# Kernel optimization log

Hardware: AMD Instinct MI355X
Metric: run time of the kernel (lower is better)

## Reference

```python
import jax, jax.numpy as jnp
import numpy as np

B, N, F = 8, 1024, 512
H, D = 4, 128  # num_heads, output_dim
LEAKY_ALPHA = 0.2
MASK_VAL = -1e10


def setup_inputs() -> dict:
    key = jax.random.key(0)
    ks = jax.random.split(key, 6)
    X = jax.random.normal(ks[0], (B, N, F), dtype=jnp.float32)
    A = (jax.random.uniform(ks[1], (B, N, N)) < 0.05).astype(jnp.float32)
    A = jnp.maximum(A, jnp.eye(N, dtype=jnp.float32)[None])
    W_att = jax.random.normal(ks[2], (H, F, D), dtype=jnp.float32) * (1.0 / np.sqrt(F))
    a_att = jax.random.normal(ks[3], (H, 2, D), dtype=jnp.float32) * (1.0 / np.sqrt(D))
    kernel = jax.random.normal(ks[4], (H, F, D), dtype=jnp.float32) * (1.0 / np.sqrt(F))
    bias = jax.random.normal(ks[5], (H * D,), dtype=jnp.float32) * 0.02
    return {"X": X, "A": A, "W_att": W_att, "a_att": a_att, "kernel": kernel, "bias": bias}


def reference(X, A, W_att, a_att, kernel, bias):
    # Per-head feature projection used only for attention scores: [H,B,N,D]
    xf = jnp.einsum('bnf,hfd->hbnd', X, W_att)
    att_self = jnp.einsum('hbnd,hd->hbn', xf, a_att[:, 0])       # [H,B,N]
    att_neigh = jnp.einsum('hbnd,hd->hbn', xf, a_att[:, 1])      # [H,B,N]
    # additive scores: scores[h,b,i,j] = self[i] + neigh[j]
    scores = att_self[..., :, None] + att_neigh[..., None, :]    # [H,B,N,N]
    scores = jnp.where(scores >= 0, scores, LEAKY_ALPHA * scores)
    scores = scores + MASK_VAL * (1.0 - A)[None]                 # adjacency mask
    attn = jax.nn.softmax(scores, axis=-1)                       # [H,B,N,N]
    # aggregate raw features X, then per-head kernel projection
    agg = jnp.einsum('hbij,bjf->hbif', attn, X)                  # [H,B,N,F]
    out = jnp.einsum('hbnf,hfd->bnhd', agg, kernel)              # [B,N,H,D]
    out = out.reshape(out.shape[0], out.shape[1], -1)            # concat heads -> [B,N,H*D]
    out = out + bias
    return jax.nn.elu(out)
```

## Files before the change

kernel.cpp:

```cpp
#include <hip/hip_runtime.h>
#include <hip/hip_bf16.h>
#include <math.h>

namespace {
constexpr int B = 8, N = 1024, F = 512, H = 4, D = 128, HD = H * D;
constexpr int ROWS = B * N;
constexpr float LEAKY = 0.2f;

constexpr size_t UV_OFF  = 0;
constexpr size_t ATT_OFF = 4096;
constexpr size_t Y_OFF   = 69632;
constexpr size_t XB_OFF  = 2166784;
constexpr size_t WKB_OFF = 4263936;
}

typedef __attribute__((ext_vector_type(8))) short short8;
typedef __attribute__((ext_vector_type(4))) float f32x4;
typedef __attribute__((ext_vector_type(2))) float f32x2;

__device__ __forceinline__ ushort bf16bits(float x) {
    __hip_bfloat16 h = __float2bfloat16(x);
    return *reinterpret_cast<ushort*>(&h);
}
__device__ __forceinline__ float blo(uint u) {
    return __uint_as_float(u << 16);
}
__device__ __forceinline__ float bhi(uint u) {
    return __uint_as_float(u & 0xffff0000u);
}

extern "C" __global__ __launch_bounds__(256) void k_pre(
    const float* __restrict__ Watt, const float* __restrict__ aatt,
    const float* __restrict__ Wk, float* __restrict__ uv,
    __hip_bfloat16* __restrict__ Wkb) {
    __shared__ ushort T[128][136];
    if (blockIdx.x < 16) {
        int h = blockIdx.x >> 2, f0 = (blockIdx.x & 3) * 128;
#pragma unroll
        for (int p = 0; p < 16; ++p) {
            int fi = p * 8 + (threadIdx.x >> 5);
            int d4 = (threadIdx.x & 31) * 4;
            float4 v = *reinterpret_cast<const float4*>(
                Wk + ((size_t)h * F + f0 + fi) * D + d4);
            T[d4 + 0][fi] = bf16bits(v.x);
            T[d4 + 1][fi] = bf16bits(v.y);
            T[d4 + 2][fi] = bf16bits(v.z);
            T[d4 + 3][fi] = bf16bits(v.w);
        }
        __syncthreads();
        int d = threadIdx.x >> 1, hf = threadIdx.x & 1;
        ushort* dst =
            (ushort*)Wkb + (size_t)(h * 128 + d) * F + f0 + hf * 64;
        const ushort* src = &T[d][hf * 64];
#pragma unroll
        for (int q = 0; q < 8; ++q)
            *reinterpret_cast<uint4*>(dst + q * 8) =
                *reinterpret_cast<const uint4*>(src + q * 8);
    } else {
        int t = (blockIdx.x - 16) * 256 + threadIdx.x;
        int f = t % F;
        int h = (t / F) % H;
        int w = t / (F * H);
        const float* Wrow = Watt + (size_t)(h * F + f) * D;
        const float* arow = aatt + (size_t)(h * 2 + w) * D;
        float s = 0.f;
#pragma unroll 4
        for (int d = 0; d < D; ++d) s = fmaf(Wrow[d], arow[d], s);
        uv[(size_t)w * (H * F) + h * F + f] = s;
    }
}

extern "C" __global__ __launch_bounds__(256) void k_att(
    const float* __restrict__ X, const float* __restrict__ uv,
    float* __restrict__ att, __hip_bfloat16* __restrict__ Xb) {
    int wave = threadIdx.x >> 6, lane = threadIdx.x & 63;
    int row = blockIdx.x * 4 + wave;
    const float4* xr = reinterpret_cast<const float4*>(X + (size_t)row * F);
    float4 v0 = xr[lane * 2], v1 = xr[lane * 2 + 1];

    union { short8 s; ushort u[8]; } pk;
    pk.u[0] = bf16bits(v0.x); pk.u[1] = bf16bits(v0.y);
    pk.u[2] = bf16bits(v0.z); pk.u[3] = bf16bits(v0.w);
    pk.u[4] = bf16bits(v1.x); pk.u[5] = bf16bits(v1.y);
    pk.u[6] = bf16bits(v1.z); pk.u[7] = bf16bits(v1.w);
    *reinterpret_cast<short8*>(Xb + (size_t)row * F + lane * 8) = pk.s;

    float acc[2][H];
#pragma unroll
    for (int w = 0; w < 2; ++w)
#pragma unroll
        for (int h = 0; h < H; ++h) {
            const float4* up = reinterpret_cast<const float4*>(
                uv + (size_t)w * (H * F) + h * F + lane * 8);
            float4 u0 = up[0], u1 = up[1];
            float a = 0.f;
            a = fmaf(v0.x, u0.x, a); a = fmaf(v0.y, u0.y, a);
            a = fmaf(v0.z, u0.z, a); a = fmaf(v0.w, u0.w, a);
            a = fmaf(v1.x, u1.x, a); a = fmaf(v1.y, u1.y, a);
            a = fmaf(v1.z, u1.z, a); a = fmaf(v1.w, u1.w, a);
            acc[w][h] = a;
        }
#pragma unroll
    for (int w = 0; w < 2; ++w)
#pragma unroll
        for (int h = 0; h < H; ++h) {
            float v = acc[w][h];
#pragma unroll
            for (int off = 32; off > 0; off >>= 1) v += __shfl_xor(v, off);
            if (lane == 0) att[(size_t)w * (H * ROWS) + h * ROWS + row] = v;
        }
}

extern "C" __global__ __launch_bounds__(256) void k_gemm(
    const __hip_bfloat16* __restrict__ Xb,
    const __hip_bfloat16* __restrict__ Wkb,
    __hip_bfloat16* __restrict__ Y) {
    __shared__ __align__(16) char smem[24576];
    int tid = threadIdx.x;
    int lane = tid & 63, wv = tid >> 6;
    int wr = wv >> 1, wc = wv & 1;
    int lt = (blockIdx.x & 7) * 64 + (blockIdx.x >> 3);
    int bm = lt >> 3, bn = lt & 7;
    int row0 = bm * 128, col0 = bn * 64;

    const ushort* Ag = (const ushort*)Xb;
    const ushort* Bg = (const ushort*)Wkb;

    int aoff[4][2], boff[2][2];
#pragma unroll
    for (int ks = 0; ks < 2; ++ks) {
        int cb = ks * 4 + (lane >> 4);
#pragma unroll
        for (int mi = 0; mi < 4; ++mi) {
            int ra = wr * 64 + mi * 16 + (lane & 15);
            aoff[mi][ks] = ra * 128 + (cb ^ (ra & 7)) * 16;
        }
#pragma unroll
        for (int ni = 0; ni < 2; ++ni) {
            int rb = wc * 32 + ni * 16 + (lane & 15);
            boff[ni][ks] = 16384 + rb * 128 + (cb ^ (rb & 7)) * 16;
        }
    }
    int srowA[4], sgbA[4], srowB[2], sgbB[2];
#pragma unroll
    for (int i = 0; i < 4; ++i) {
        srowA[i] = i * 32 + wv * 8 + (lane >> 3);
        sgbA[i] = (lane & 7) ^ (srowA[i] & 7);
    }
#pragma unroll
    for (int i = 0; i < 2; ++i) {
        srowB[i] = i * 32 + wv * 8 + (lane >> 3);
        sgbB[i] = (lane & 7) ^ (srowB[i] & 7);
    }

    f32x4 acc[4][2] = {};
    for (int k0 = 0; k0 < F; k0 += 64) {
        __syncthreads();
#pragma unroll
        for (int i = 0; i < 4; ++i) {
            const ushort* ga = Ag + (size_t)(row0 + srowA[i]) * F + k0 + sgbA[i] * 8;
            __builtin_amdgcn_global_load_lds(
                (const __attribute__((address_space(1))) uint32_t*)ga,
                (__attribute__((address_space(3))) uint32_t*)(smem + i * 4096 + wv * 1024),
                16, 0, 0);
        }
#pragma unroll
        for (int i = 0; i < 2; ++i) {
            const ushort* gb = Bg + (size_t)(col0 + srowB[i]) * F + k0 + sgbB[i] * 8;
            __builtin_amdgcn_global_load_lds(
                (const __attribute__((address_space(1))) uint32_t*)gb,
                (__attribute__((address_space(3))) uint32_t*)(smem + 16384 + i * 4096 + wv * 1024),
                16, 0, 0);
        }
        __syncthreads();
#pragma unroll
        for (int ks = 0; ks < 2; ++ks) {
            short8 af[4], bf[2];
#pragma unroll
            for (int mi = 0; mi < 4; ++mi)
                af[mi] = *reinterpret_cast<short8*>(smem + aoff[mi][ks]);
#pragma unroll
            for (int ni = 0; ni < 2; ++ni)
                bf[ni] = *reinterpret_cast<short8*>(smem + boff[ni][ks]);
#pragma unroll
            for (int mi = 0; mi < 4; ++mi)
#pragma unroll
                for (int ni = 0; ni < 2; ++ni)
                    acc[mi][ni] = __builtin_amdgcn_mfma_f32_16x16x32_bf16(
                        af[mi], bf[ni], acc[mi][ni], 0, 0, 0);
        }
    }
    int cr = (lane >> 4) * 4, cc = lane & 15;
#pragma unroll
    for (int mi = 0; mi < 4; ++mi)
#pragma unroll
        for (int ni = 0; ni < 2; ++ni) {
            int gr = row0 + wr * 64 + mi * 16 + cr;
            int gc = col0 + wc * 32 + ni * 16 + cc;
#pragma unroll
            for (int r = 0; r < 4; ++r)
                Y[(size_t)(gr + r) * HD + gc] =
                    __float2bfloat16(acc[mi][ni][r]);
        }
}

extern "C" __global__ __launch_bounds__(256) void k_attn_agg(
    const float* __restrict__ A, const float* __restrict__ att,
    const ushort* __restrict__ Y, const float* __restrict__ bias,
    float* __restrict__ out) {
    int g = blockIdx.x;
    int bi = ((g & 7) << 10) | (g >> 3);
    int b = bi >> 10;
    int tid = threadIdx.x;
    int lane = tid & 63, wv = tid >> 6;
    __shared__ int idxs[N];
    __shared__ int2 ent[H][64];
    __shared__ int wsum[4];

    const float* Arow = A + (size_t)bi * N;
    float4 av = *reinterpret_cast<const float4*>(Arow + tid * 4);
    int cnt = (av.x != 0.f) + (av.y != 0.f) + (av.z != 0.f) + (av.w != 0.f);
    int isc = cnt;
#pragma unroll
    for (int off = 1; off < 64; off <<= 1) {
        int t = __shfl_up(isc, off);
        if (lane >= off) isc += t;
    }
    if (lane == 63) wsum[wv] = isc;
    __syncthreads();
    int prefix = 0;
#pragma unroll
    for (int wj = 0; wj < 4; ++wj) prefix += (wj < wv) ? wsum[wj] : 0;
    int nnz = wsum[0] + wsum[1] + wsum[2] + wsum[3];
    int wo = prefix + isc - cnt;
    int jb = tid * 4;
    if (av.x != 0.f) idxs[wo++] = jb;
    if (av.y != 0.f) idxs[wo++] = jb + 1;
    if (av.z != 0.f) idxs[wo++] = jb + 2;
    if (av.w != 0.f) idxs[wo++] = jb + 3;
    __syncthreads();

    int h = wv;
    int grp = lane >> 4, sub = lane & 15;
    const float* nrow = att + (size_t)(H + h) * ROWS + (size_t)b * N;
    float sself = att[(size_t)h * ROWS + bi];
    float sb = sself + 16.f;
    float m = fmaxf(sb, LEAKY * sb);

    const char* Ybyte = (const char*)(Y + ((size_t)b * N) * HD + h * D + sub * 8);
    float lsum = 0.f;
    f32x2 acc2[4] = {};
    for (int c0 = 0; c0 < nnz; c0 += 64) {
        int cn = min(64, nnz - c0);
        int idx = 0;
        float e = 0.f;
        if (lane < cn) {
            idx = idxs[c0 + lane];
            float s = sself + nrow[idx];
            s = fmaxf(s, LEAKY * s);
            e = __expf(s - m);
        }
        lsum += e;
        ent[h][lane] = make_int2(idx << 10, __float_as_int(e));
        asm volatile("s_waitcnt lgkmcnt(0)" ::: "memory");
        int kpad = (cn + 15) & ~15;
        for (int k = 0; k < kpad; k += 16) {
            int2 p[4];
#pragma unroll
            for (int q = 0; q < 4; ++q) p[q] = ent[h][k + q * 4 + grp];
            uint4 y[4];
#pragma unroll
            for (int q = 0; q < 4; ++q)
                y[q] = *reinterpret_cast<const uint4*>(
                    Ybyte + (size_t)(uint)p[q].x);
#pragma unroll
            for (int q = 0; q < 4; ++q) {
                float w = __int_as_float(p[q].y);
                f32x2 w2 = {w, w};
                acc2[0] = __builtin_elementwise_fma(
                    w2, (f32x2){blo(y[q].x), bhi(y[q].x)}, acc2[0]);
                acc2[1] = __builtin_elementwise_fma(
                    w2, (f32x2){blo(y[q].y), bhi(y[q].y)}, acc2[1]);
                acc2[2] = __builtin_elementwise_fma(
                    w2, (f32x2){blo(y[q].z), bhi(y[q].z)}, acc2[2]);
                acc2[3] = __builtin_elementwise_fma(
                    w2, (f32x2){blo(y[q].w), bhi(y[q].w)}, acc2[3]);
            }
        }
    }
#pragma unroll
    for (int off = 32; off > 0; off >>= 1) lsum += __shfl_xor(lsum, off);
#pragma unroll
    for (int q = 0; q < 4; ++q) {
        acc2[q].x += __shfl_xor(acc2[q].x, 16);
        acc2[q].x += __shfl_xor(acc2[q].x, 32);
        acc2[q].y += __shfl_xor(acc2[q].y, 16);
        acc2[q].y += __shfl_xor(acc2[q].y, 32);
    }
    if (grp == 0) {
        float inv = 1.f / lsum;
        int cbase = h * D + sub * 8;
        float4 b0 = *reinterpret_cast<const float4*>(bias + cbase);
        float4 b1 = *reinterpret_cast<const float4*>(bias + cbase + 4);
        float o[8];
        o[0] = acc2[0].x * inv + b0.x; o[1] = acc2[0].y * inv + b0.y;
        o[2] = acc2[1].x * inv + b0.z; o[3] = acc2[1].y * inv + b0.w;
        o[4] = acc2[2].x * inv + b1.x; o[5] = acc2[2].y * inv + b1.y;
        o[6] = acc2[3].x * inv + b1.z; o[7] = acc2[3].y * inv + b1.w;
#pragma unroll
        for (int q = 0; q < 8; ++q)
            o[q] = o[q] > 0.f ? o[q] : (__expf(o[q]) - 1.f);
        float* op = out + (size_t)bi * HD + cbase;
        *reinterpret_cast<float4*>(op) = make_float4(o[0], o[1], o[2], o[3]);
        *reinterpret_cast<float4*>(op + 4) = make_float4(o[4], o[5], o[6], o[7]);
    }
}

extern "C" void kernel_launch(void* const* d_in, const int* in_sizes, int n_in,
                              void* d_out, int out_size, void* d_ws,
                              size_t ws_size, hipStream_t stream) {
    const float* X    = (const float*)d_in[0];
    const float* A    = (const float*)d_in[1];
    const float* Watt = (const float*)d_in[2];
    const float* aatt = (const float*)d_in[3];
    const float* Wk   = (const float*)d_in[4];
    const float* bias = (const float*)d_in[5];
    float* out = (float*)d_out;
    float* ws  = (float*)d_ws;

    float* uv  = ws + UV_OFF;
    float* att = ws + ATT_OFF;
    __hip_bfloat16* Yb  = (__hip_bfloat16*)(ws + Y_OFF);
    __hip_bfloat16* Xb  = (__hip_bfloat16*)(ws + XB_OFF);
    __hip_bfloat16* Wkb = (__hip_bfloat16*)(ws + WKB_OFF);

    hipLaunchKernelGGL(k_pre, dim3(32), dim3(256), 0, stream, Watt, aatt, Wk,
                       uv, Wkb);
    hipLaunchKernelGGL(k_att, dim3(ROWS / 4), dim3(256), 0, stream, X, uv, att, Xb);
    hipLaunchKernelGGL(k_gemm, dim3((ROWS / 128) * (HD / 64)), dim3(256), 0,
                       stream, Xb, Wkb, Yb);
    hipLaunchKernelGGL(k_attn_agg, dim3(ROWS), dim3(256), 0, stream, A, att,
                       (const ushort*)Yb, bias, out);
}
```

Baseline: 61.63 us.

## Stage gathered Y rows into LDS via async double-buffered global_load_lds

The neighbour-feature gather in the attention aggregation kernel now uses asynchronous global-to-LDS loads into a per-wave double buffer. Two 16-neighbour slots are issued ahead, and the next slot is prefetched while the current one is consumed. Softmax weights move to a separate LDS array, and score loads overlap with the first gathers. The goal is to hide gather latency and lift memory-level parallelism. The cost is extra LDS (32 KB per block), possible occupancy loss, and manual vmcnt bookkeeping that could race when a buffer is overwritten.

Measured after the change: 75.21 us. 22.0% more time.

```diff
diff --git a/kernel.cpp b/kernel.cpp
--- a/kernel.cpp
+++ b/kernel.cpp
@@ -214,8 +214,9 @@
     int tid = threadIdx.x;
     int lane = tid & 63, wv = tid >> 6;
     __shared__ int idxs[N];
-    __shared__ int2 ent[H][64];
+    __shared__ float wts[4][64];
     __shared__ int wsum[4];
+    __shared__ __align__(16) char stage[4][2][4096];
 
     const float* Arow = A + (size_t)bi * N;
     float4 av = *reinterpret_cast<const float4*>(Arow + tid * 4);
@@ -244,50 +245,75 @@
     int grp = lane >> 4, sub = lane & 15;
     const float* nrow = att + (size_t)(H + h) * ROWS + (size_t)b * N;
     float sself = att[(size_t)h * ROWS + bi];
-    float sb = sself + 16.f;
-    float m = fmaxf(sb, LEAKY * sb);
-
-    const char* Ybyte = (const char*)(Y + ((size_t)b * N) * HD + h * D + sub * 8);
+    float sbv = sself + 16.f;
+    float m = fmaxf(sbv, LEAKY * sbv);
+
+    const char* Ybatch = (const char*)(Y + ((size_t)b * N) * HD);
+    int hsub = h * 256 + sub * 16;
+
+#define ISSUE_SLOT(S, SLOT)                                                  \
+    {                                                                        \
+        _Pragma("unroll") for (int gq = 0; gq < 4; ++gq) {                   \
+            int kq = c0 + (S) * 16 + gq * 4 + grp;                           \
+            int kk = kq < nnz ? kq : 0;                                      \
+            int ix = idxs[kk];                                               \
+            const char* srcp = Ybatch + (size_t)(uint)(ix << 10) + hsub;     \
+            __builtin_amdgcn_global_load_lds(                                \
+                (const __attribute__((address_space(1))) uint32_t*)srcp,     \
+                (__attribute__((address_space(3))) uint32_t*)(               \
+                    &stage[wv][SLOT][gq * 1024]),                            \
+                16, 0, 0);                                                   \
+        }                                                                    \
+    }
+
     float lsum = 0.f;
     f32x2 acc2[4] = {};
     for (int c0 = 0; c0 < nnz; c0 += 64) {
         int cn = min(64, nnz - c0);
-        int idx = 0;
+        int nst = (cn + 15) >> 4;
+        int idx0 = 0;
+        float sraw = 0.f;
+        if (lane < cn) {
+            idx0 = idxs[c0 + lane];
+            sraw = nrow[idx0];
+        }
+        ISSUE_SLOT(0, 0);
+        if (nst > 1) ISSUE_SLOT(1, 1);
         float e = 0.f;
         if (lane < cn) {
-            idx = idxs[c0 + lane];
-            float s = sself + nrow[idx];
+            float s = sself + sraw;
             s = fmaxf(s, LEAKY * s);
             e = __expf(s - m);
         }
         lsum += e;
-        ent[h][lane] = make_int2(idx << 10, __float_as_int(e));
+        wts[wv][lane] = e;
         asm volatile("s_waitcnt lgkmcnt(0)" ::: "memory");
-        int kpad = (cn + 15) & ~15;
-        for (int k = 0; k < kpad; k += 16) {
-            int2 p[4];
-#pragma unroll
-            for (int q = 0; q < 4; ++q) p[q] = ent[h][k + q * 4 + grp];
-            uint4 y[4];
-#pragma unroll
-            for (int q = 0; q < 4; ++q)
-                y[q] = *reinterpret_cast<const uint4*>(
-                    Ybyte + (size_t)(uint)p[q].x);
-#pragma unroll
-            for (int q = 0; q < 4; ++q) {
-                float w = __int_as_float(p[q].y);
+        for (int s = 0; s < nst; ++s) {
+            if (s < nst - 1)
+                asm volatile("s_waitcnt vmcnt(4)" ::: "memory");
+            else
+                asm volatile("s_waitcnt vmcnt(0)" ::: "memory");
+            const char* sbase = stage[wv][s & 1];
+#pragma unroll
+            for (int t = 0; t < 4; ++t) {
+                int n = 4 * t + grp;
+                uint4 y = *reinterpret_cast<const uint4*>(
+                    sbase + n * 256 + sub * 16);
+                float w = wts[wv][s * 16 + n];
                 f32x2 w2 = {w, w};
                 acc2[0] = __builtin_elementwise_fma(
-                    w2, (f32x2){blo(y[q].x), bhi(y[q].x)}, acc2[0]);
+                    w2, (f32x2){blo(y.x), bhi(y.x)}, acc2[0]);
                 acc2[1] = __builtin_elementwise_fma(
-                    w2, (f32x2){blo(y[q].y), bhi(y[q].y)}, acc2[1]);
+                    w2, (f32x2){blo(y.y), bhi(y.y)}, acc2[1]);
                 acc2[2] = __builtin_elementwise_fma(
-                    w2, (f32x2){blo(y[q].z), bhi(y[q].z)}, acc2[2]);
+                    w2, (f32x2){blo(y.z), bhi(y.z)}, acc2[2]);
                 acc2[3] = __builtin_elementwise_fma(
-                    w2, (f32x2){blo(y[q].w), bhi(y[q].w)}, acc2[3]);
+                    w2, (f32x2){blo(y.w), bhi(y.w)}, acc2[3]);
             }
-        }
-    }
+            if (s + 2 < nst) ISSUE_SLOT(s + 2, s & 1);
+        }
+    }
+#undef ISSUE_SLOT
 #pragma unroll
     for (int off = 32; off > 0; off >>= 1) lsum += __shfl_xor(lsum, off);
 #pragma unroll
```

## Split each head's neighbor aggregation across two wavefronts with LDS reduction

Applied to the files above, without the earlier changes.

The attention-aggregation kernel now launches 512 threads per row, so each head gets two wavefronts. Each wavefront handles 32 neighbors of every 64-neighbor chunk. Partial accumulators and softmax sums are combined through shared memory before the final bias and ELU step. This doubles memory-level parallelism on the sparse gathered rows. The cost is an extra block barrier, LDS traffic, and half-idle lanes during score computation.

Result: slower. 72.53 us (+17.7%).

```diff
diff --git a/kernel.cpp b/kernel.cpp
--- a/kernel.cpp
+++ b/kernel.cpp
@@ -204,7 +204,7 @@
         }
 }
 
-extern "C" __global__ __launch_bounds__(256) void k_attn_agg(
+extern "C" __global__ __launch_bounds__(512) void k_attn_agg(
     const float* __restrict__ A, const float* __restrict__ att,
     const ushort* __restrict__ Y, const float* __restrict__ bias,
     float* __restrict__ out) {
@@ -214,12 +214,14 @@
     int tid = threadIdx.x;
     int lane = tid & 63, wv = tid >> 6;
     __shared__ int idxs[N];
-    __shared__ int2 ent[H][64];
-    __shared__ int wsum[4];
+    __shared__ int2 ent[8][32];
+    __shared__ float part[8][16][8];
+    __shared__ float lsums[8];
+    __shared__ int wsum[8];
 
     const float* Arow = A + (size_t)bi * N;
-    float4 av = *reinterpret_cast<const float4*>(Arow + tid * 4);
-    int cnt = (av.x != 0.f) + (av.y != 0.f) + (av.z != 0.f) + (av.w != 0.f);
+    float2 av = *reinterpret_cast<const float2*>(Arow + tid * 2);
+    int cnt = (av.x != 0.f) + (av.y != 0.f);
     int isc = cnt;
 #pragma unroll
     for (int off = 1; off < 64; off <<= 1) {
@@ -228,19 +230,19 @@
     }
     if (lane == 63) wsum[wv] = isc;
     __syncthreads();
-    int prefix = 0;
-#pragma unroll
-    for (int wj = 0; wj < 4; ++wj) prefix += (wj < wv) ? wsum[wj] : 0;
-    int nnz = wsum[0] + wsum[1] + wsum[2] + wsum[3];
+    int prefix = 0, nnz = 0;
+#pragma unroll
+    for (int wj = 0; wj < 8; ++wj) {
+        prefix += (wj < wv) ? wsum[wj] : 0;
+        nnz += wsum[wj];
+    }
     int wo = prefix + isc - cnt;
-    int jb = tid * 4;
+    int jb = tid * 2;
     if (av.x != 0.f) idxs[wo++] = jb;
     if (av.y != 0.f) idxs[wo++] = jb + 1;
-    if (av.z != 0.f) idxs[wo++] = jb + 2;
-    if (av.w != 0.f) idxs[wo++] = jb + 3;
     __syncthreads();
 
-    int h = wv;
+    int h = wv >> 1, half = wv & 1;
     int grp = lane >> 4, sub = lane & 15;
     const float* nrow = att + (size_t)(H + h) * ROWS + (size_t)b * N;
     float sself = att[(size_t)h * ROWS + bi];
@@ -251,23 +253,26 @@
     float lsum = 0.f;
     f32x2 acc2[4] = {};
     for (int c0 = 0; c0 < nnz; c0 += 64) {
-        int cn = min(64, nnz - c0);
+        int base = c0 + 32 * half;
+        int cn = nnz - base;
+        cn = cn < 0 ? 0 : (cn > 32 ? 32 : cn);
         int idx = 0;
         float e = 0.f;
         if (lane < cn) {
-            idx = idxs[c0 + lane];
+            idx = idxs[base + lane];
             float s = sself + nrow[idx];
             s = fmaxf(s, LEAKY * s);
             e = __expf(s - m);
         }
         lsum += e;
-        ent[h][lane] = make_int2(idx << 10, __float_as_int(e));
+        if (lane < 32)
+            ent[wv][lane] = make_int2(idx << 10, __float_as_int(e));
         asm volatile("s_waitcnt lgkmcnt(0)" ::: "memory");
         int kpad = (cn + 15) & ~15;
         for (int k = 0; k < kpad; k += 16) {
             int2 p[4];
 #pragma unroll
-            for (int q = 0; q < 4; ++q) p[q] = ent[h][k + q * 4 + grp];
+            for (int q = 0; q < 4; ++q) p[q] = ent[wv][k + q * 4 + grp];
             uint4 y[4];
 #pragma unroll
             for (int q = 0; q < 4; ++q)
@@ -298,21 +303,24 @@
         acc2[q].y += __shfl_xor(acc2[q].y, 32);
     }
     if (grp == 0) {
-        float inv = 1.f / lsum;
-        int cbase = h * D + sub * 8;
-        float4 b0 = *reinterpret_cast<const float4*>(bias + cbase);
-        float4 b1 = *reinterpret_cast<const float4*>(bias + cbase + 4);
-        float o[8];
-        o[0] = acc2[0].x * inv + b0.x; o[1] = acc2[0].y * inv + b0.y;
-        o[2] = acc2[1].x * inv + b0.z; o[3] = acc2[1].y * inv + b0.w;
-        o[4] = acc2[2].x * inv + b1.x; o[5] = acc2[2].y * inv + b1.y;
-        o[6] = acc2[3].x * inv + b1.z; o[7] = acc2[3].y * inv + b1.w;
-#pragma unroll
-        for (int q = 0; q < 8; ++q)
-            o[q] = o[q] > 0.f ? o[q] : (__expf(o[q]) - 1.f);
-        float* op = out + (size_t)bi * HD + cbase;
-        *reinterpret_cast<float4*>(op) = make_float4(o[0], o[1], o[2], o[3]);
-        *reinterpret_cast<float4*>(op + 4) = make_float4(o[4], o[5], o[6], o[7]);
+#pragma unroll
+        for (int q = 0; q < 4; ++q) {
+            part[wv][sub][2 * q] = acc2[q].x;
+            part[wv][sub][2 * q + 1] = acc2[q].y;
+        }
+    }
+    if (lane == 0) lsums[wv] = lsum;
+    __syncthreads();
+
+    {
+        int s = tid;
+        int hh = s >> 7, d = s & 127;
+        int sb2 = d >> 3, q = d & 7;
+        float v = part[2 * hh][sb2][q] + part[2 * hh + 1][sb2][q];
+        float inv = 1.f / (lsums[2 * hh] + lsums[2 * hh + 1]);
+        float o = v * inv + bias[s];
+        o = o > 0.f ? o : (__expf(o) - 1.f);
+        out[(size_t)bi * HD + s] = o;
     }
 }
 
@@ -339,6 +347,6 @@
     hipLaunchKernelGGL(k_att, dim3(ROWS / 4), dim3(256), 0, stream, X, uv, att, Xb);
     hipLaunchKernelGGL(k_gemm, dim3((ROWS / 128) * (HD / 64)), dim3(256), 0,
                        stream, Xb, Wkb, Yb);
-    hipLaunchKernelGGL(k_attn_agg, dim3(ROWS), dim3(256), 0, stream, A, att,
+    hipLaunchKernelGGL(k_attn_agg, dim3(ROWS), dim3(512), 0, stream, A, att,
                        (const ushort*)Yb, bias, out);
 }
```
